# Kernel optimization log

Measured on AMD Instinct MI355X. Metric: run time of the kernel, lower is better.

## Reference

```python
import jax, jax.numpy as jnp
import numpy as np

D_MODEL = 1024
N_HEADS = 16
D_HEAD = D_MODEL // N_HEADS
B, S = 2, 2048


def setup_inputs() -> dict:
    key = jax.random.key(0)
    ks = jax.random.split(key, 7)
    query = jax.random.normal(ks[0], (B, S, D_MODEL), dtype=jnp.float32)
    k_in = jax.random.normal(ks[1], (B, S, D_MODEL), dtype=jnp.float32)
    v_in = jax.random.normal(ks[2], (B, S, D_MODEL), dtype=jnp.float32)
    # causal mask: True = attend allowed (torch code keeps where mask != 0)
    mask = jnp.tril(jnp.ones((S, S), dtype=bool))
    scale = 1.0 / np.sqrt(D_MODEL)
    Wq = jax.random.normal(ks[3], (D_MODEL, D_MODEL), dtype=jnp.float32) * scale
    Wk = jax.random.normal(ks[4], (D_MODEL, D_MODEL), dtype=jnp.float32) * scale
    Wv = jax.random.normal(ks[5], (D_MODEL, D_MODEL), dtype=jnp.float32) * scale
    Wo = jax.random.normal(ks[6], (D_MODEL, D_MODEL), dtype=jnp.float32) * scale
    return {"query": query, "key": k_in, "value": v_in, "mask": mask,
            "Wq": Wq, "Wk": Wk, "Wv": Wv, "Wo": Wo}


def reference(query, key, value, mask, Wq, Wk, Wv, Wo):
    b, sq, d = query.shape
    # bias-free linear: x @ W.T (torch nn.Linear convention)
    q = (query @ Wq.T).reshape(b, sq, N_HEADS, D_HEAD).transpose(0, 2, 1, 3)  # b h s d
    k = (key @ Wk.T).reshape(b, -1, N_HEADS, D_HEAD).transpose(0, 2, 1, 3)
    v = (value @ Wv.T).reshape(b, -1, N_HEADS, D_HEAD).transpose(0, 2, 1, 3)
    scores = jnp.einsum('bhqd,bhkd->bhqk', q, k) / jnp.sqrt(jnp.float32(D_HEAD))
    scores = jnp.where(mask[None, None, :, :], scores, jnp.float32(-1e9))
    attn = jax.nn.softmax(scores, axis=-1)
    # dropout is identity in eval mode
    ctx = jnp.einsum('bhqk,bhkd->bhqd', attn, v)
    ctx = ctx.transpose(0, 2, 1, 3).reshape(b, sq, d)
    return ctx @ Wo.T
```

## Files before the change

kernel.cpp:

```cpp
#include <hip/hip_runtime.h>
#include <hip/hip_bf16.h>
#include <cstdint>


typedef unsigned short u16;
typedef u16 u16x4 __attribute__((ext_vector_type(4)));
typedef u16 u16x8 __attribute__((ext_vector_type(8)));
typedef unsigned u32x4 __attribute__((ext_vector_type(4)));
typedef __bf16 bf16x8 __attribute__((ext_vector_type(8)));
typedef float f32x4 __attribute__((ext_vector_type(4)));

#define S_LEN 2048
#define DM 1024
#define NH 16
#define DH 64
#define BATCH 2
#define MTOT (BATCH*S_LEN)

__device__ __forceinline__ u16 f2bf(float f) {
  union { float f; unsigned u; } v; v.f = f;
  unsigned r = v.u + 0x7FFFu + ((v.u >> 16) & 1u);
  return (u16)(r >> 16);
}

__device__ __forceinline__ f32x4 mfma16(u16x8 a, u16x8 b, f32x4 c) {
  return __builtin_amdgcn_mfma_f32_16x16x32_bf16(
      __builtin_bit_cast(bf16x8, a), __builtin_bit_cast(bf16x8, b), c, 0, 0, 0);
}
__device__ __forceinline__ unsigned cvtpk_bf16(float lo, float hi) {
  unsigned r;
  asm("v_cvt_pk_bf16_f32 %0, %1, %2" : "=v"(r) : "v"(lo), "v"(hi));
  return r;
}
__device__ __forceinline__ void gload16(const u16* g, u16* l) {
  __builtin_amdgcn_global_load_lds(
      (const __attribute__((address_space(1))) unsigned int*)g,
      (__attribute__((address_space(3))) unsigned int*)l, 16, 0, 0);
}

__global__ __launch_bounds__(256) void cvt_kernel(
    const float* __restrict__ s0, const float* __restrict__ s1,
    const float* __restrict__ s2, const float* __restrict__ s3,
    const float* __restrict__ s4, const float* __restrict__ s5,
    const float* __restrict__ s6,
    u16* __restrict__ d0, u16* __restrict__ d1, u16* __restrict__ d2,
    u16* __restrict__ d3, u16* __restrict__ d4, u16* __restrict__ d5,
    u16* __restrict__ d6) {
  const int y = blockIdx.y;
  const float* s; u16* d; int n;
  switch (y) {
    case 0: s = s0; d = d0; n = MTOT*DM; break;
    case 1: s = s1; d = d1; n = MTOT*DM; break;
    case 2: s = s2; d = d2; n = MTOT*DM; break;
    case 3: s = s3; d = d3; n = DM*DM;   break;
    case 4: s = s4; d = d4; n = DM*DM;   break;
    case 5: s = s5; d = d5; n = DM*DM;   break;
    default: s = s6; d = d6; n = DM*DM;  break;
  }
  int i = (blockIdx.x * 256 + threadIdx.x) * 4;
  if (i >= n) return;
  f32x4 v = *(const f32x4*)&s[i];
  u16x4 o;
  o[0] = f2bf(v[0]); o[1] = f2bf(v[1]); o[2] = f2bf(v[2]); o[3] = f2bf(v[3]);
  *(u16x4*)&d[i] = o;
}

#define BM 128
#define BN 128
#define BKK 32

template<int MODE>
__device__ __forceinline__ void gemm_core(const u16* __restrict__ A,
                                          const u16* __restrict__ Bw,
                                          void* __restrict__ Cv,
                                          int K, float scale) {
  __shared__ u16 As[BM * BKK];
  __shared__ u16 Bs[BN * BKK];
  const int tid  = threadIdx.x;
  const int lane = tid & 63, w = tid >> 6;
  const int g = lane >> 4, r16 = lane & 15;
  const int wm = w >> 1, wn = w & 1;
  const int rowBase = blockIdx.y * BM;
  const int colBase = blockIdx.x * BN;
  f32x4 acc[4][4] = {};
  const int srow = lane >> 2;
  const int skc  = (lane & 3) * 8;
  const u16* gA[2]; const u16* gB[2]; u16* lA[2]; u16* lB[2];
#pragma unroll
  for (int j = 0; j < 2; j++) {
    const int c = w * 2 + j;
    gA[j] = &A [(size_t)(rowBase + c * 16 + srow) * K + skc];
    gB[j] = &Bw[(size_t)(colBase + c * 16 + srow) * K + skc];
    lA[j] = &As[c * 512];
    lB[j] = &Bs[c * 512];
  }
  for (int k0 = 0; k0 < K; k0 += BKK) {
    __syncthreads();
#pragma unroll
    for (int j = 0; j < 2; j++) {
      gload16(gA[j] + k0, lA[j]);
      gload16(gB[j] + k0, lB[j]);
    }
    __syncthreads();
    u16x8 af[4], bfv[4];
#pragma unroll
    for (int i = 0; i < 4; i++) af[i]  = *(const u16x8*)&As[(wm*64 + i*16 + r16) * BKK + g*8];
#pragma unroll
    for (int j = 0; j < 4; j++) bfv[j] = *(const u16x8*)&Bs[(wn*64 + j*16 + r16) * BKK + g*8];
    __builtin_amdgcn_s_setprio(1);
#pragma unroll
    for (int i = 0; i < 4; i++)
#pragma unroll
      for (int j = 0; j < 4; j++) acc[i][j] = mfma16(af[i], bfv[j], acc[i][j]);
    __builtin_amdgcn_s_setprio(0);
  }
#pragma unroll
  for (int i = 0; i < 4; i++) {
#pragma unroll
    for (int j = 0; j < 4; j++) {
      int row = rowBase + wm*64 + i*16 + 4*g;
      int col = colBase + wn*64 + j*16 + r16;
      if (MODE == 0) {
        u16* O = (u16*)Cv;
        int head = col >> 6, d = col & 63;
#pragma unroll
        for (int r = 0; r < 4; r++)
          O[((size_t)head * MTOT + row + r) * DH + d] = f2bf(acc[i][j][r] * scale);
      } else if (MODE == 1) {
        u16x4 o;
#pragma unroll
        for (int r = 0; r < 4; r++) o[r] = f2bf(acc[i][j][r]);
        *(u16x4*)&((u16*)Cv)[(size_t)col * MTOT + row] = o;
      } else {
#pragma unroll
        for (int r = 0; r < 4; r++)
          ((float*)Cv)[(size_t)(row + r) * DM + col] = acc[i][j][r];
      }
    }
  }
}

__global__ __launch_bounds__(256) void qkv_proj_kernel(
    const u16* __restrict__ Xq, const u16* __restrict__ Xk, const u16* __restrict__ Xv,
    const u16* __restrict__ Wq, const u16* __restrict__ Wk, const u16* __restrict__ Wv,
    u16* __restrict__ Qp, u16* __restrict__ Kp, u16* __restrict__ Vt) {
  const int z = blockIdx.z;
  if (z == 0)      gemm_core<0>(Xq, Wq, Qp, DM, 0.125f * 1.44269504f);
  else if (z == 1) gemm_core<0>(Xk, Wk, Kp, DM, 1.0f);
  else             gemm_core<1>(Xv, Wv, Vt, DM, 1.0f);
}

__global__ __launch_bounds__(256) void out_proj_kernel(
    const u16* __restrict__ Ctx, const u16* __restrict__ Wo, float* __restrict__ Out) {
  gemm_core<2>(Ctx, Wo, Out, DM, 1.0f);
}


#define STAGE(B, T)                                                            \
  {                                                                            \
    const int kv0_ = (T) * 64;                                                 \
    _Pragma("unroll")                                                          \
    for (int j = 0; j < 2; j++) {                                              \
      const int rb = wv * 16 + j * 8;                                          \
      gload16(&Kbase[(size_t)(kv0_ + rb + srow) * DH + sc16 * 8],              \
              &Kl[B][rb * 64]);                                                \
      gload16(&Vbase[(size_t)(rb + srow) * MTOT + kv0_ + sc16 * 8],            \
              &Vl[B][rb * 64]);                                                \
    }                                                                          \
  }

#define TILE_BODY(BUF, T)                                                      \
  {                                                                            \
    const int kv0 = (T) * 64;                                                  \
    f32x4 s[4] = {};                                                           \
    __builtin_amdgcn_s_setprio(1);                                             \
    _Pragma("unroll")                                                          \
    for (int f = 0; f < 4; f++) {                                              \
      _Pragma("unroll")                                                        \
      for (int ds = 0; ds < 2; ds++) {                                         \
        u16x8 kf = *(const u16x8*)&Kl[BUF][(f * 16 + q16) * 64 +               \
                                           ((ds * 4 + g) ^ qx7) * 8];          \
        s[f] = mfma16(kf, qf[ds], s[f]);                                       \
      }                                                                        \
    }                                                                          \
    __builtin_amdgcn_s_setprio(0);                                             \
    if ((T) == ntb - 1) {             \
      const int qg = qb16 + q16;                                               \
      _Pragma("unroll")                                                        \
      for (int f = 0; f < 4; f++)                                              \
        _Pragma("unroll")                                                      \
        for (int r = 0; r < 4; r++)                                            \
          if (kv0 + f * 16 + 4 * g + r > qg) s[f][r] = -1e30f;                 \
    }                                                                          \
    float mx[4];                                                               \
    _Pragma("unroll")                                                          \
    for (int r = 0; r < 4; r++)                                                \
      mx[r] = fmaxf(fmaxf(s[0][r], s[1][r]), fmaxf(s[2][r], s[3][r]));         \
    float pmax = fmaxf(fmaxf(mx[0], mx[1]), fmaxf(mx[2], mx[3]));              \
    pmax = fmaxf(pmax, __shfl_xor(pmax, 16, 64));                              \
    pmax = fmaxf(pmax, __shfl_xor(pmax, 32, 64));                              \
    if (__ballot(pmax > m + 11.5f)) {              \
      float mnew = fmaxf(m, pmax);                                             \
      float alpha = exp2f(m - mnew);                                           \
      l *= alpha; m = mnew;                                                    \
      float fsc[4];                                                            \
      _Pragma("unroll")                                                        \
      for (int r = 0; r < 4; r++) fsc[r] = __shfl(alpha, 4 * g + r, 64);       \
      _Pragma("unroll")                                                        \
      for (int dt = 0; dt < 4; dt++)                                           \
        _Pragma("unroll")                                                      \
        for (int r = 0; r < 4; r++) ctx[dt][r] *= fsc[r];                      \
    }                                                                          \
    _Pragma("unroll")                                                          \
    for (int f = 0; f < 4; f++)                                                \
      _Pragma("unroll")                                                        \
      for (int r = 0; r < 4; r++) s[f][r] = exp2f(s[f][r] - m);                \
    f32x4 sv = (s[0] + s[1]) + (s[2] + s[3]);                                  \
    float psum = (sv[0] + sv[1]) + (sv[2] + sv[3]);                            \
    psum += __shfl_xor(psum, 16, 64);                                          \
    psum += __shfl_xor(psum, 32, 64);                                          \
    l += psum;                                                                 \
            \
    _Pragma("unroll")                                                          \
    for (int f = 0; f < 4; f++) {                                              \
      const int cidx = (((2 * f + (g >> 1)) ^ qx7) * 8) + 4 * (g & 1);         \
      *(unsigned*)&P16[q16 * 64 + cidx]     = cvtpk_bf16(s[f][0], s[f][1]);    \
      *(unsigned*)&P16[q16 * 64 + cidx + 2] = cvtpk_bf16(s[f][2], s[f][3]);    \
    }                                                                          \
    asm volatile("s_waitcnt lgkmcnt(0)" ::: "memory");                         \
    __builtin_amdgcn_sched_barrier(0);                                         \
    u16x8 pa0 = *(const u16x8*)&P16[q16 * 64 + ((g)     ^ qx7) * 8];           \
    u16x8 pa1 = *(const u16x8*)&P16[q16 * 64 + ((4 + g) ^ qx7) * 8];           \
    __builtin_amdgcn_s_setprio(1);                                             \
    _Pragma("unroll")                                                          \
    for (int dt = 0; dt < 4; dt++) {                                           \
      u16x8 vf0 = *(const u16x8*)&Vl[BUF][(dt * 16 + q16) * 64 +               \
                                          ((g)     ^ qx7) * 8];                \
      u16x8 vf1 = *(const u16x8*)&Vl[BUF][(dt * 16 + q16) * 64 +               \
                                          ((4 + g) ^ qx7) * 8];                \
      ctx[dt] = mfma16(pa0, vf0, ctx[dt]);                                     \
      ctx[dt] = mfma16(pa1, vf1, ctx[dt]);                                     \
    }                                                                          \
    __builtin_amdgcn_s_setprio(0);                                             \
  }

__global__ __launch_bounds__(256, 4) void attn_kernel(const u16* __restrict__ Qp,
                                                      const u16* __restrict__ Kp,
                                                      const u16* __restrict__ Vt,
                                                      u16* __restrict__ Ctx) {
  __shared__ u16 Kl[2][64 * 64];
  __shared__ u16 Vl[2][64 * 64];
  __shared__ u16 Pl[4][16 * 64];
  const int tid = threadIdx.x;
  const int lane = tid & 63, wv = tid >> 6;
  const int q16 = lane & 15, g = lane >> 4;
  const int qx7 = q16 & 7;
  const int flat = blockIdx.x;
  const int xcd = flat & 7, idx = flat >> 3;
  const int bh = xcd * 4 + (idx & 3);
  const int qc = 31 - (idx >> 2);
  const int bb = bh >> 4, h = bh & 15;
  const int qb16 = qc * 64 + wv * 16;

  const u16* Qbase = Qp + (size_t)(h * MTOT + bb * S_LEN) * DH;
  const u16* Kbase = Kp + (size_t)(h * MTOT + bb * S_LEN) * DH;
  const u16* Vbase = Vt + (size_t)(h * DH) * MTOT + bb * S_LEN;
  u16* P16 = Pl[wv];

  u16x8 qf[2];
#pragma unroll
  for (int ds = 0; ds < 2; ds++)
    qf[ds] = *(const u16x8*)&Qbase[(size_t)(qb16 + q16) * DH + ds * 32 + g * 8];

  f32x4 ctx[4] = {};
  float m = -3.0e38f, l = 0.f;
  const int ntb = qc + 1;

  const int srow = lane >> 3;
  const int sc16 = (lane & 7) ^ srow;

  STAGE(0, 0);
  int cur = 0;
  for (int t = 0; t < ntb; ++t) {
    __syncthreads();
    if (t + 1 < ntb) STAGE(cur ^ 1, t + 1);
    TILE_BODY(cur, t);
    cur ^= 1;
  }

  const float linv = 1.f / l;
  float flv[4];
#pragma unroll
  for (int r = 0; r < 4; r++) flv[r] = __shfl(linv, 4 * g + r, 64);
#pragma unroll
  for (int dt = 0; dt < 4; dt++)
#pragma unroll
    for (int r = 0; r < 4; r++) {
      size_t grow = (size_t)(bb * S_LEN + qb16 + 4 * g + r) * DM + h * DH;
      Ctx[grow + dt * 16 + q16] = f2bf(ctx[dt][r] * flv[r]);
    }
}

extern "C" void kernel_launch(void* const* d_in, const int* in_sizes, int n_in,
                              void* d_out, int out_size, void* d_ws, size_t ws_size,
                              hipStream_t stream) {
  const float* q_in = (const float*)d_in[0];
  const float* k_in = (const float*)d_in[1];
  const float* v_in = (const float*)d_in[2];
  const float* wq = (const float*)d_in[4];
  const float* wk = (const float*)d_in[5];
  const float* wv = (const float*)d_in[6];
  const float* wo = (const float*)d_in[7];

  char* ws = (char*)d_ws;
  const size_t MB = 1024ull * 1024ull;
  u16* Qp  = (u16*)(ws + 0  * MB);
  u16* Kp  = (u16*)(ws + 8  * MB);
  u16* Vt  = (u16*)(ws + 16 * MB);
  u16* Ctx = (u16*)(ws + 24 * MB);
  u16* Xq  = (u16*)(ws + 32 * MB);
  u16* Xk  = (u16*)(ws + 40 * MB);
  u16* Xv  = (u16*)(ws + 48 * MB);
  u16* Wqb = (u16*)(ws + 56 * MB);
  u16* Wkb = (u16*)(ws + 58 * MB);
  u16* Wvb = (u16*)(ws + 60 * MB);
  u16* Wob = (u16*)(ws + 62 * MB);

  cvt_kernel<<<dim3(4096, 7, 1), 256, 0, stream>>>(
      q_in, k_in, v_in, wq, wk, wv, wo, Xq, Xk, Xv, Wqb, Wkb, Wvb, Wob);
  qkv_proj_kernel<<<dim3(DM / BN, MTOT / BM, 3), 256, 0, stream>>>(
      Xq, Xk, Xv, Wqb, Wkb, Wvb, Qp, Kp, Vt);
  attn_kernel<<<dim3(1024), 256, 0, stream>>>(Qp, Kp, Vt, Ctx);
  out_proj_kernel<<<dim3(DM / BN, MTOT / BM), 256, 0, stream>>>(Ctx, Wob, (float*)d_out);
}
```

Baseline: 130.0 us.

## Fuse fp32-to-bf16 activation conversion into QKV projection GEMM loads

Removes the separate conversion pass over the three large activation tensors. The QKV GEMM now loads fp32 activations directly into LDS with an XOR swizzle and converts them to bf16 when building MFMA fragments. The weight conversion kernel is shrunk to only the four weight matrices. The attention P store is also merged into a single 64-bit write. The cost is double the LDS traffic and footprint for the A tile, plus extra conversion work inside the GEMM inner loop.

```diff
diff --git a/kernel.cpp b/kernel.cpp
--- a/kernel.cpp
+++ b/kernel.cpp
@@ -6,6 +6,7 @@
 typedef unsigned short u16;
 typedef u16 u16x4 __attribute__((ext_vector_type(4)));
 typedef u16 u16x8 __attribute__((ext_vector_type(8)));
+typedef unsigned u32x2 __attribute__((ext_vector_type(2)));
 typedef unsigned u32x4 __attribute__((ext_vector_type(4)));
 typedef __bf16 bf16x8 __attribute__((ext_vector_type(8)));
 typedef float f32x4 __attribute__((ext_vector_type(4)));
@@ -41,24 +42,12 @@
 __global__ __launch_bounds__(256) void cvt_kernel(
     const float* __restrict__ s0, const float* __restrict__ s1,
     const float* __restrict__ s2, const float* __restrict__ s3,
-    const float* __restrict__ s4, const float* __restrict__ s5,
-    const float* __restrict__ s6,
-    u16* __restrict__ d0, u16* __restrict__ d1, u16* __restrict__ d2,
-    u16* __restrict__ d3, u16* __restrict__ d4, u16* __restrict__ d5,
-    u16* __restrict__ d6) {
+    u16* __restrict__ d0, u16* __restrict__ d1,
+    u16* __restrict__ d2, u16* __restrict__ d3) {
   const int y = blockIdx.y;
-  const float* s; u16* d; int n;
-  switch (y) {
-    case 0: s = s0; d = d0; n = MTOT*DM; break;
-    case 1: s = s1; d = d1; n = MTOT*DM; break;
-    case 2: s = s2; d = d2; n = MTOT*DM; break;
-    case 3: s = s3; d = d3; n = DM*DM;   break;
-    case 4: s = s4; d = d4; n = DM*DM;   break;
-    case 5: s = s5; d = d5; n = DM*DM;   break;
-    default: s = s6; d = d6; n = DM*DM;  break;
-  }
+  const float* s = (y == 0) ? s0 : (y == 1) ? s1 : (y == 2) ? s2 : s3;
+  u16* d       = (y == 0) ? d0 : (y == 1) ? d1 : (y == 2) ? d2 : d3;
   int i = (blockIdx.x * 256 + threadIdx.x) * 4;
-  if (i >= n) return;
   f32x4 v = *(const f32x4*)&s[i];
   u16x4 o;
   o[0] = f2bf(v[0]); o[1] = f2bf(v[1]); o[2] = f2bf(v[2]); o[3] = f2bf(v[3]);
@@ -69,13 +58,16 @@
 #define BN 128
 #define BKK 32
 
-template<int MODE>
-__device__ __forceinline__ void gemm_core(const u16* __restrict__ A,
+template<int MODE, bool AF32>
+__device__ __forceinline__ void gemm_core(const void* __restrict__ Av,
                                           const u16* __restrict__ Bw,
                                           void* __restrict__ Cv,
                                           int K, float scale) {
-  __shared__ u16 As[BM * BKK];
+  __shared__ u16 As[AF32 ? BM * BKK * 2 : BM * BKK];
   __shared__ u16 Bs[BN * BKK];
+  float* As32 = (float*)As;
+  const u16* A16 = (const u16*)Av;
+  const float* A32 = (const float*)Av;
   const int tid  = threadIdx.x;
   const int lane = tid & 63, w = tid >> 6;
   const int g = lane >> 4, r16 = lane & 15;
@@ -83,28 +75,65 @@
   const int rowBase = blockIdx.y * BM;
   const int colBase = blockIdx.x * BN;
   f32x4 acc[4][4] = {};
-  const int srow = lane >> 2;
-  const int skc  = (lane & 3) * 8;
-  const u16* gA[2]; const u16* gB[2]; u16* lA[2]; u16* lB[2];
+
+  const int srowB = lane >> 2;
+  const int skcB  = (lane & 3) * 8;
+  const u16* gB[2]; u16* lB[2];
 #pragma unroll
   for (int j = 0; j < 2; j++) {
     const int c = w * 2 + j;
-    gA[j] = &A [(size_t)(rowBase + c * 16 + srow) * K + skc];
-    gB[j] = &Bw[(size_t)(colBase + c * 16 + srow) * K + skc];
-    lA[j] = &As[c * 512];
+    gB[j] = &Bw[(size_t)(colBase + c * 16 + srowB) * K + skcB];
     lB[j] = &Bs[c * 512];
   }
+  const u16* gA16[2]; u16* lA16[2];
+  const float* gA32[4]; float* lA32[4];
+  if constexpr (AF32) {
+    const int srow8 = lane >> 3;
+    const int scF   = ((lane & 7) ^ srow8) * 4;
+#pragma unroll
+    for (int j = 0; j < 4; j++) {
+      const int rb = w * 32 + j * 8;
+      gA32[j] = &A32[(size_t)(rowBase + rb + srow8) * K + scF];
+      lA32[j] = &As32[rb * 32];
+    }
+  } else {
+#pragma unroll
+    for (int j = 0; j < 2; j++) {
+      const int c = w * 2 + j;
+      gA16[j] = &A16[(size_t)(rowBase + c * 16 + srowB) * K + skcB];
+      lA16[j] = &As[c * 512];
+    }
+  }
+
   for (int k0 = 0; k0 < K; k0 += BKK) {
     __syncthreads();
-#pragma unroll
-    for (int j = 0; j < 2; j++) {
-      gload16(gA[j] + k0, lA[j]);
-      gload16(gB[j] + k0, lB[j]);
-    }
+    if constexpr (AF32) {
+#pragma unroll
+      for (int j = 0; j < 4; j++) gload16((const u16*)(gA32[j] + k0), (u16*)lA32[j]);
+    } else {
+#pragma unroll
+      for (int j = 0; j < 2; j++) gload16(gA16[j] + k0, lA16[j]);
+    }
+#pragma unroll
+    for (int j = 0; j < 2; j++) gload16(gB[j] + k0, lB[j]);
     __syncthreads();
     u16x8 af[4], bfv[4];
-#pragma unroll
-    for (int i = 0; i < 4; i++) af[i]  = *(const u16x8*)&As[(wm*64 + i*16 + r16) * BKK + g*8];
+    if constexpr (AF32) {
+      const int rx = r16 & 7;
+#pragma unroll
+      for (int i = 0; i < 4; i++) {
+        const int base = (wm * 64 + i * 16 + r16) * 32;
+        f32x4 a0 = *(const f32x4*)&As32[base + (((g * 2)     ^ rx) * 4)];
+        f32x4 a1 = *(const f32x4*)&As32[base + (((g * 2 + 1) ^ rx) * 4)];
+        u32x4 wv = {cvtpk_bf16(a0[0], a0[1]), cvtpk_bf16(a0[2], a0[3]),
+                    cvtpk_bf16(a1[0], a1[1]), cvtpk_bf16(a1[2], a1[3])};
+        af[i] = __builtin_bit_cast(u16x8, wv);
+      }
+    } else {
+#pragma unroll
+      for (int i = 0; i < 4; i++)
+        af[i] = *(const u16x8*)&As[(wm*64 + i*16 + r16) * BKK + g*8];
+    }
 #pragma unroll
     for (int j = 0; j < 4; j++) bfv[j] = *(const u16x8*)&Bs[(wn*64 + j*16 + r16) * BKK + g*8];
     __builtin_amdgcn_s_setprio(1);
@@ -141,18 +170,18 @@
 }
 
 __global__ __launch_bounds__(256) void qkv_proj_kernel(
-    const u16* __restrict__ Xq, const u16* __restrict__ Xk, const u16* __restrict__ Xv,
+    const float* __restrict__ Xq, const float* __restrict__ Xk, const float* __restrict__ Xv,
     const u16* __restrict__ Wq, const u16* __restrict__ Wk, const u16* __restrict__ Wv,
     u16* __restrict__ Qp, u16* __restrict__ Kp, u16* __restrict__ Vt) {
   const int z = blockIdx.z;
-  if (z == 0)      gemm_core<0>(Xq, Wq, Qp, DM, 0.125f * 1.44269504f);
-  else if (z == 1) gemm_core<0>(Xk, Wk, Kp, DM, 1.0f);
-  else             gemm_core<1>(Xv, Wv, Vt, DM, 1.0f);
+  if (z == 0)      gemm_core<0, true>(Xq, Wq, Qp, DM, 0.125f * 1.44269504f);
+  else if (z == 1) gemm_core<0, true>(Xk, Wk, Kp, DM, 1.0f);
+  else             gemm_core<1, true>(Xv, Wv, Vt, DM, 1.0f);
 }
 
 __global__ __launch_bounds__(256) void out_proj_kernel(
     const u16* __restrict__ Ctx, const u16* __restrict__ Wo, float* __restrict__ Out) {
-  gemm_core<2>(Ctx, Wo, Out, DM, 1.0f);
+  gemm_core<2, false>(Ctx, Wo, Out, DM, 1.0f);
 }
 
 
@@ -224,8 +253,8 @@
     _Pragma("unroll")                                                          \
     for (int f = 0; f < 4; f++) {                                              \
       const int cidx = (((2 * f + (g >> 1)) ^ qx7) * 8) + 4 * (g & 1);         \
-      *(unsigned*)&P16[q16 * 64 + cidx]     = cvtpk_bf16(s[f][0], s[f][1]);    \
-      *(unsigned*)&P16[q16 * 64 + cidx + 2] = cvtpk_bf16(s[f][2], s[f][3]);    \
+      u32x2 pw = {cvtpk_bf16(s[f][0], s[f][1]), cvtpk_bf16(s[f][2], s[f][3])}; \
+      *(u32x2*)&P16[q16 * 64 + cidx] = pw;                                     \
     }                                                                          \
     asm volatile("s_waitcnt lgkmcnt(0)" ::: "memory");                         \
     __builtin_amdgcn_sched_barrier(0);                                         \
@@ -318,18 +347,15 @@
   u16* Kp  = (u16*)(ws + 8  * MB);
   u16* Vt  = (u16*)(ws + 16 * MB);
   u16* Ctx = (u16*)(ws + 24 * MB);
-  u16* Xq  = (u16*)(ws + 32 * MB);
-  u16* Xk  = (u16*)(ws + 40 * MB);
-  u16* Xv  = (u16*)(ws + 48 * MB);
   u16* Wqb = (u16*)(ws + 56 * MB);
   u16* Wkb = (u16*)(ws + 58 * MB);
   u16* Wvb = (u16*)(ws + 60 * MB);
   u16* Wob = (u16*)(ws + 62 * MB);
 
-  cvt_kernel<<<dim3(4096, 7, 1), 256, 0, stream>>>(
-      q_in, k_in, v_in, wq, wk, wv, wo, Xq, Xk, Xv, Wqb, Wkb, Wvb, Wob);
+  cvt_kernel<<<dim3(DM * DM / 1024, 4), 256, 0, stream>>>(
+      wq, wk, wv, wo, Wqb, Wkb, Wvb, Wob);
   qkv_proj_kernel<<<dim3(DM / BN, MTOT / BM, 3), 256, 0, stream>>>(
-      Xq, Xk, Xv, Wqb, Wkb, Wvb, Qp, Kp, Vt);
+      q_in, k_in, v_in, Wqb, Wkb, Wvb, Qp, Kp, Vt);
   attn_kernel<<<dim3(1024), 256, 0, stream>>>(Qp, Kp, Vt, Ctx);
   out_proj_kernel<<<dim3(DM / BN, MTOT / BM), 256, 0, stream>>>(Ctx, Wob, (float*)d_out);
 }
```

New measurement: 144.6 us. 11.2% more time.
